# Performance work log

Hardware: AMD Instinct MI355X
Metric: run time of the kernel (lower is better)

## Reference

```python
import jax, jax.numpy as jnp
import numpy as np

N, F_IN, H, W = 8192, 512, 256, 64
THRESHOLD = 0.8


def setup_inputs() -> dict:
    key = jax.random.key(0)
    ks = jax.random.split(key, 9)
    def lin(k, fan_in, shape):
        return (jax.random.normal(k, shape, jnp.float32) / np.sqrt(fan_in)).astype(jnp.float32)
    return {
        "state_batch": jax.random.normal(ks[0], (N, F_IN), jnp.float32),
        "W1": lin(ks[1], F_IN, (F_IN, H)), "b1": jnp.zeros((H,), jnp.float32),
        "W2": lin(ks[2], H, (H, H)),      "b2": jnp.zeros((H,), jnp.float32),
        "Wq": lin(ks[3], H, (H, W)),      "bq": jnp.zeros((W,), jnp.float32),
        "Wh": lin(ks[4], W, (W, 1)),      "bh": jnp.zeros((1,), jnp.float32),
    }


def reference(state_batch, W1, b1, W2, b2, Wq, bq, Wh, bh):
    # classical encoder: two ReLU Linear layers
    enc = jax.nn.relu(state_batch @ W1 + b1)
    enc = jax.nn.relu(enc @ W2 + b2)
    # quantum layer surrogate: bounded features in [-1, 1] like PauliZ expectations
    q_out = jnp.tanh(enc @ Wq + bq)                      # [N, W]

    # pairwise squared-cosine fidelity (vectorized Gram matrix, replaces
    # the itertools.combinations + .item() host-sync loop)
    qn = q_out / (jnp.linalg.norm(q_out, axis=1, keepdims=True) + 1e-12)
    fid = (qn @ qn.T) ** 2                               # [N, N]

    n = q_out.shape[0]
    # graph edges: fid >= threshold, no self loops; edge weight = 1.0
    mask = (fid >= THRESHOLD) & (~jnp.eye(n, dtype=bool))
    deg = mask.sum(axis=1)
    wsum = mask.astype(q_out.dtype).sum(axis=1)          # all weights are 1.0
    # mean neighbor weight; nodes with no neighbors keep their own feature (factor 1)
    mean_w = jnp.where(deg > 0, wsum / jnp.maximum(deg, 1).astype(q_out.dtype), 1.0)
    attn = q_out * mean_w[:, None]                       # [N, W]

    agg = attn.sum(axis=0, keepdims=True)                # [1, W]
    out = (agg @ Wh + bh).squeeze(-1)                    # [1]
    return out
```

## Files before the change

### kernel.cpp

```cpp
#include <hip/hip_runtime.h>
#include <hip/hip_bf16.h>
#include <math.h>


#define N_ROWS 8192
#define F_IN   512
#define H_DIM  256
#define W_DIM  64

#define LDS_S 520
#define LDE   264

#define W1_FRAGS (16 * 16 * 64)
#define W2_FRAGS (16 * 8 * 64)
#define WQ_FRAGS (4 * 8 * 64)
#define PREP_T   (W1_FRAGS + W2_FRAGS + WQ_FRAGS)
#define PREP_BLOCKS ((PREP_T + 255) / 256)

using bf16x8 = __attribute__((ext_vector_type(8))) short;
using bf16x4 = __attribute__((ext_vector_type(4))) short;
using f32x4  = __attribute__((ext_vector_type(4))) float;
typedef __hip_bfloat16 bf16;

__device__ __forceinline__ void split2(float v, bf16& hi, bf16& lo) {
    bf16 h = __float2bfloat16(v);
    hi = h;
    lo = __float2bfloat16(v - __bfloat162float(h));
}

__global__ __launch_bounds__(256) void prep_w(
    const float* __restrict__ W1, const float* __restrict__ W2,
    const float* __restrict__ Wq, const float* __restrict__ bh,
    bf16* __restrict__ W1h, bf16* __restrict__ W1l,
    bf16* __restrict__ W2h, bf16* __restrict__ W2l,
    bf16* __restrict__ Wqh, bf16* __restrict__ Wql,
    float* __restrict__ out)
{
    if (blockIdx.x == 0 && threadIdx.x == 0) out[0] = bh[0];
    int gid = blockIdx.x * 256 + threadIdx.x;
    if (gid < W1_FRAGS) {
        const int l = gid & 63, ks = (gid >> 6) & 15, n16 = gid >> 10;
        const int n = n16 * 16 + (l & 15);
        const int kb = ks * 32 + ((l >> 4) << 3);
        bf16 hb[8], lb[8];
        #pragma unroll
        for (int j = 0; j < 8; ++j)
            split2(W1[(size_t)(kb + j) * H_DIM + n], hb[j], lb[j]);
        *(bf16x8*)(W1h + (size_t)gid * 8) = *(const bf16x8*)hb;
        *(bf16x8*)(W1l + (size_t)gid * 8) = *(const bf16x8*)lb;
        return;
    }
    gid -= W1_FRAGS;
    if (gid < W2_FRAGS) {
        const int l = gid & 63, ks = (gid >> 6) & 7, n16 = gid >> 9;
        const int n = n16 * 16 + (l & 15);
        const int kb = ks * 32 + ((l >> 4) << 3);
        bf16 hb[8], lb[8];
        #pragma unroll
        for (int j = 0; j < 8; ++j)
            split2(W2[(size_t)(kb + j) * H_DIM + n], hb[j], lb[j]);
        *(bf16x8*)(W2h + (size_t)gid * 8) = *(const bf16x8*)hb;
        *(bf16x8*)(W2l + (size_t)gid * 8) = *(const bf16x8*)lb;
        return;
    }
    gid -= W2_FRAGS;
    if (gid < WQ_FRAGS) {
        const int l = gid & 63, ks = (gid >> 6) & 7, n16 = gid >> 9;
        const int n = n16 * 16 + (l & 15);
        const int kb = ks * 32 + ((l >> 4) << 3);
        bf16 hb[8], lb[8];
        #pragma unroll
        for (int j = 0; j < 8; ++j)
            split2(Wq[(size_t)(kb + j) * W_DIM + n], hb[j], lb[j]);
        *(bf16x8*)(Wqh + (size_t)gid * 8) = *(const bf16x8*)hb;
        *(bf16x8*)(Wql + (size_t)gid * 8) = *(const bf16x8*)lb;
    }
}

__global__ __launch_bounds__(512) void fused_chain(
    const float* __restrict__ S,
    const bf16* __restrict__ W1h, const bf16* __restrict__ W1l,
    const bf16* __restrict__ W2h, const bf16* __restrict__ W2l,
    const bf16* __restrict__ Wqh, const bf16* __restrict__ Wql,
    const float* __restrict__ b1, const float* __restrict__ b2,
    const float* __restrict__ bq, const float* __restrict__ Wh,
    float* __restrict__ out)
{
    __shared__ bf16 Ssh[32 * LDS_S];
    __shared__ bf16 Ssl[32 * LDS_S];
    __shared__ bf16 E1h[32 * LDE];
    __shared__ bf16 E1l[32 * LDE];
    __shared__ bf16 E2h[32 * LDE];
    __shared__ bf16 E2l[32 * LDE];
    __shared__ float red[2][64];

    const int t = threadIdx.x;
    const int lane = t & 63;
    const int w = t >> 6, quad = lane >> 4, m16 = t & 15;
    const int row0 = blockIdx.x * 32;

    #pragma unroll
    for (int i = 0; i < 8; ++i) {
        const int idx = i * 2048 + t * 4;
        const int r = idx >> 9, c = idx & 511;
        float4 sv = *(const float4*)(S + (size_t)(row0 + r) * F_IN + c);
        bf16 hb[4], lb[4];
        split2(sv.x, hb[0], lb[0]); split2(sv.y, hb[1], lb[1]);
        split2(sv.z, hb[2], lb[2]); split2(sv.w, hb[3], lb[3]);
        *(bf16x4*)&Ssh[r * LDS_S + c] = *(const bf16x4*)hb;
        *(bf16x4*)&Ssl[r * LDS_S + c] = *(const bf16x4*)lb;
    }

    f32x4 acc[2][2] = {};
    {
        bf16x8 rh[4][2], rl[4][2];
        #pragma unroll
        for (int p = 0; p < 3; ++p)
            #pragma unroll
            for (int jj = 0; jj < 2; ++jj) {
                const size_t off = ((size_t)(((2 * w + jj) * 16 + p) * 64 + lane)) * 8;
                rh[p][jj] = *(const bf16x8*)(W1h + off);
                rl[p][jj] = *(const bf16x8*)(W1l + off);
            }
        __syncthreads();
        #pragma unroll
        for (int ks = 0; ks < 16; ++ks) {
            const int cur = ks & 3;
            if (ks + 3 < 16) {
                const int nx = (ks + 3) & 3;
                #pragma unroll
                for (int jj = 0; jj < 2; ++jj) {
                    const size_t off = ((size_t)(((2 * w + jj) * 16 + ks + 3) * 64 + lane)) * 8;
                    rh[nx][jj] = *(const bf16x8*)(W1h + off);
                    rl[nx][jj] = *(const bf16x8*)(W1l + off);
                }
            }
            const int ao = ks * 32 + quad * 8;
            bf16x8 a0h = *(const bf16x8*)&Ssh[m16 * LDS_S + ao];
            bf16x8 a0l = *(const bf16x8*)&Ssl[m16 * LDS_S + ao];
            bf16x8 a1h = *(const bf16x8*)&Ssh[(16 + m16) * LDS_S + ao];
            bf16x8 a1l = *(const bf16x8*)&Ssl[(16 + m16) * LDS_S + ao];
            #pragma unroll
            for (int jj = 0; jj < 2; ++jj) {
                bf16x8 b_h = rh[cur][jj], b_l = rl[cur][jj];
                acc[0][jj] = __builtin_amdgcn_mfma_f32_16x16x32_bf16(a0h, b_h, acc[0][jj], 0, 0, 0);
                acc[0][jj] = __builtin_amdgcn_mfma_f32_16x16x32_bf16(a0l, b_h, acc[0][jj], 0, 0, 0);
                acc[0][jj] = __builtin_amdgcn_mfma_f32_16x16x32_bf16(a0h, b_l, acc[0][jj], 0, 0, 0);
                acc[1][jj] = __builtin_amdgcn_mfma_f32_16x16x32_bf16(a1h, b_h, acc[1][jj], 0, 0, 0);
                acc[1][jj] = __builtin_amdgcn_mfma_f32_16x16x32_bf16(a1l, b_h, acc[1][jj], 0, 0, 0);
                acc[1][jj] = __builtin_amdgcn_mfma_f32_16x16x32_bf16(a1h, b_l, acc[1][jj], 0, 0, 0);
            }
        }
    }
    #pragma unroll
    for (int i = 0; i < 2; ++i)
        #pragma unroll
        for (int jj = 0; jj < 2; ++jj) {
            const int c = 32 * w + jj * 16 + m16;
            const float bv = b1[c];
            #pragma unroll
            for (int r = 0; r < 4; ++r) {
                const int rr = i * 16 + quad * 4 + r;
                float vv = fmaxf(acc[i][jj][r] + bv, 0.0f);
                split2(vv, E1h[rr * LDE + c], E1l[rr * LDE + c]);
            }
        }

    {
        bf16x8 rh[4][2], rl[4][2];
        #pragma unroll
        for (int p = 0; p < 3; ++p)
            #pragma unroll
            for (int jj = 0; jj < 2; ++jj) {
                const size_t off = ((size_t)(((2 * w + jj) * 8 + p) * 64 + lane)) * 8;
                rh[p][jj] = *(const bf16x8*)(W2h + off);
                rl[p][jj] = *(const bf16x8*)(W2l + off);
            }
        __syncthreads();
        #pragma unroll
        for (int i = 0; i < 2; ++i)
            #pragma unroll
            for (int jj = 0; jj < 2; ++jj)
                acc[i][jj] = (f32x4){0.f, 0.f, 0.f, 0.f};
        #pragma unroll
        for (int ks = 0; ks < 8; ++ks) {
            const int cur = ks & 3;
            if (ks + 3 < 8) {
                const int nx = (ks + 3) & 3;
                #pragma unroll
                for (int jj = 0; jj < 2; ++jj) {
                    const size_t off = ((size_t)(((2 * w + jj) * 8 + ks + 3) * 64 + lane)) * 8;
                    rh[nx][jj] = *(const bf16x8*)(W2h + off);
                    rl[nx][jj] = *(const bf16x8*)(W2l + off);
                }
            }
            const int ao = ks * 32 + quad * 8;
            bf16x8 a0h = *(const bf16x8*)&E1h[m16 * LDE + ao];
            bf16x8 a0l = *(const bf16x8*)&E1l[m16 * LDE + ao];
            bf16x8 a1h = *(const bf16x8*)&E1h[(16 + m16) * LDE + ao];
            bf16x8 a1l = *(const bf16x8*)&E1l[(16 + m16) * LDE + ao];
            #pragma unroll
            for (int jj = 0; jj < 2; ++jj) {
                bf16x8 b_h = rh[cur][jj], b_l = rl[cur][jj];
                acc[0][jj] = __builtin_amdgcn_mfma_f32_16x16x32_bf16(a0h, b_h, acc[0][jj], 0, 0, 0);
                acc[0][jj] = __builtin_amdgcn_mfma_f32_16x16x32_bf16(a0l, b_h, acc[0][jj], 0, 0, 0);
                acc[0][jj] = __builtin_amdgcn_mfma_f32_16x16x32_bf16(a0h, b_l, acc[0][jj], 0, 0, 0);
                acc[1][jj] = __builtin_amdgcn_mfma_f32_16x16x32_bf16(a1h, b_h, acc[1][jj], 0, 0, 0);
                acc[1][jj] = __builtin_amdgcn_mfma_f32_16x16x32_bf16(a1l, b_h, acc[1][jj], 0, 0, 0);
                acc[1][jj] = __builtin_amdgcn_mfma_f32_16x16x32_bf16(a1h, b_l, acc[1][jj], 0, 0, 0);
            }
        }
    }
    #pragma unroll
    for (int i = 0; i < 2; ++i)
        #pragma unroll
        for (int jj = 0; jj < 2; ++jj) {
            const int c = 32 * w + jj * 16 + m16;
            const float bv = b2[c];
            #pragma unroll
            for (int r = 0; r < 4; ++r) {
                const int rr = i * 16 + quad * 4 + r;
                float vv = fmaxf(acc[i][jj][r] + bv, 0.0f);
                split2(vv, E2h[rr * LDE + c], E2l[rr * LDE + c]);
            }
        }

    {
        const int rf = w >> 2, cf = w & 3;
        bf16x8 rh[4], rl[4];
        #pragma unroll
        for (int p = 0; p < 3; ++p) {
            const size_t off = ((size_t)((cf * 8 + p) * 64 + lane)) * 8;
            rh[p] = *(const bf16x8*)(Wqh + off);
            rl[p] = *(const bf16x8*)(Wql + off);
        }
        __syncthreads();
        f32x4 acc3 = {0.f, 0.f, 0.f, 0.f};
        #pragma unroll
        for (int ks = 0; ks < 8; ++ks) {
            const int cur = ks & 3;
            if (ks + 3 < 8) {
                const int nx = (ks + 3) & 3;
                const size_t off = ((size_t)((cf * 8 + ks + 3) * 64 + lane)) * 8;
                rh[nx] = *(const bf16x8*)(Wqh + off);
                rl[nx] = *(const bf16x8*)(Wql + off);
            }
            const int ao = ks * 32 + quad * 8;
            bf16x8 a_h = *(const bf16x8*)&E2h[(rf * 16 + m16) * LDE + ao];
            bf16x8 a_l = *(const bf16x8*)&E2l[(rf * 16 + m16) * LDE + ao];
            acc3 = __builtin_amdgcn_mfma_f32_16x16x32_bf16(a_h, rh[cur], acc3, 0, 0, 0);
            acc3 = __builtin_amdgcn_mfma_f32_16x16x32_bf16(a_l, rh[cur], acc3, 0, 0, 0);
            acc3 = __builtin_amdgcn_mfma_f32_16x16x32_bf16(a_h, rl[cur], acc3, 0, 0, 0);
        }
        const int c = cf * 16 + m16;
        const float bv = bq[c];
        float v = 0.f;
        #pragma unroll
        for (int r = 0; r < 4; ++r)
            v += tanhf(acc3[r] + bv);
        v += __shfl_xor(v, 16, 64);
        v += __shfl_xor(v, 32, 64);
        if (quad == 0) red[rf][c] = v;
        __syncthreads();
        if (t < W_DIM) {
            float s = (red[0][t] + red[1][t]) * Wh[t];
            #pragma unroll
            for (int o = 32; o > 0; o >>= 1) s += __shfl_down(s, o);
            if (t == 0) atomicAdd(out, s);
        }
    }
}

extern "C" void kernel_launch(void* const* d_in, const int* in_sizes, int n_in,
                              void* d_out, int out_size, void* d_ws, size_t ws_size,
                              hipStream_t stream) {
    const float* state = (const float*)d_in[0];
    const float* W1    = (const float*)d_in[1];
    const float* b1    = (const float*)d_in[2];
    const float* W2    = (const float*)d_in[3];
    const float* b2    = (const float*)d_in[4];
    const float* Wq    = (const float*)d_in[5];
    const float* bq    = (const float*)d_in[6];
    const float* Wh    = (const float*)d_in[7];
    const float* bh    = (const float*)d_in[8];

    bf16* p = (bf16*)d_ws;
    bf16* W1h = p; p += (size_t)H_DIM * F_IN;
    bf16* W1l = p; p += (size_t)H_DIM * F_IN;
    bf16* W2h = p; p += (size_t)H_DIM * H_DIM;
    bf16* W2l = p; p += (size_t)H_DIM * H_DIM;
    bf16* Wqh = p; p += (size_t)W_DIM * H_DIM;
    bf16* Wql = p; p += (size_t)W_DIM * H_DIM;

    prep_w<<<PREP_BLOCKS, 256, 0, stream>>>(
        W1, W2, Wq, bh, W1h, W1l, W2h, W2l, Wqh, Wql, (float*)d_out);

    fused_chain<<<N_ROWS / 32, 512, 0, stream>>>(
        state, W1h, W1l, W2h, W2l, Wqh, Wql, b1, b2, bq, Wh, (float*)d_out);
}
```

Before: 96.18 us.

## Split input staging in two halves to overlap conversion with first-layer MFMAs

The state tile is now loaded into registers up front, and the hi/lo split into LDS happens in two column halves. The first half is written before the first barrier. The second half is converted and stored right after that barrier, and the first eight k-steps of the W1 GEMM run on the first half before a second barrier. The aim is to hide global-load latency and conversion work behind MFMA work. The cost is an extra barrier and higher register pressure from holding 8 float4 values.

```diff
diff --git a/kernel.cpp b/kernel.cpp
--- a/kernel.cpp
+++ b/kernel.cpp
@@ -99,16 +99,18 @@
     const int w = t >> 6, quad = lane >> 4, m16 = t & 15;
     const int row0 = blockIdx.x * 32;
 
+    float4 va[4], vb[4];
     #pragma unroll
-    for (int i = 0; i < 8; ++i) {
-        const int idx = i * 2048 + t * 4;
-        const int r = idx >> 9, c = idx & 511;
-        float4 sv = *(const float4*)(S + (size_t)(row0 + r) * F_IN + c);
-        bf16 hb[4], lb[4];
-        split2(sv.x, hb[0], lb[0]); split2(sv.y, hb[1], lb[1]);
-        split2(sv.z, hb[2], lb[2]); split2(sv.w, hb[3], lb[3]);
-        *(bf16x4*)&Ssh[r * LDS_S + c] = *(const bf16x4*)hb;
-        *(bf16x4*)&Ssl[r * LDS_S + c] = *(const bf16x4*)lb;
+    for (int i = 0; i < 4; ++i) {
+        const int idx2 = i * 512 + t;
+        const int r = idx2 >> 6, c = (idx2 & 63) << 2;
+        va[i] = *(const float4*)(S + (size_t)(row0 + r) * F_IN + c);
+    }
+    #pragma unroll
+    for (int i = 0; i < 4; ++i) {
+        const int idx2 = i * 512 + t;
+        const int r = idx2 >> 6, c = 256 + ((idx2 & 63) << 2);
+        vb[i] = *(const float4*)(S + (size_t)(row0 + r) * F_IN + c);
     }
 
     f32x4 acc[2][2] = {};
@@ -122,9 +124,58 @@
                 rh[p][jj] = *(const bf16x8*)(W1h + off);
                 rl[p][jj] = *(const bf16x8*)(W1l + off);
             }
-        __syncthreads();
-        #pragma unroll
-        for (int ks = 0; ks < 16; ++ks) {
+        #pragma unroll
+        for (int i = 0; i < 4; ++i) {
+            const int idx2 = i * 512 + t;
+            const int r = idx2 >> 6, c = (idx2 & 63) << 2;
+            bf16 hb[4], lb[4];
+            split2(va[i].x, hb[0], lb[0]); split2(va[i].y, hb[1], lb[1]);
+            split2(va[i].z, hb[2], lb[2]); split2(va[i].w, hb[3], lb[3]);
+            *(bf16x4*)&Ssh[r * LDS_S + c] = *(const bf16x4*)hb;
+            *(bf16x4*)&Ssl[r * LDS_S + c] = *(const bf16x4*)lb;
+        }
+        __syncthreads();
+        #pragma unroll
+        for (int i = 0; i < 4; ++i) {
+            const int idx2 = i * 512 + t;
+            const int r = idx2 >> 6, c = 256 + ((idx2 & 63) << 2);
+            bf16 hb[4], lb[4];
+            split2(vb[i].x, hb[0], lb[0]); split2(vb[i].y, hb[1], lb[1]);
+            split2(vb[i].z, hb[2], lb[2]); split2(vb[i].w, hb[3], lb[3]);
+            *(bf16x4*)&Ssh[r * LDS_S + c] = *(const bf16x4*)hb;
+            *(bf16x4*)&Ssl[r * LDS_S + c] = *(const bf16x4*)lb;
+        }
+        #pragma unroll
+        for (int ks = 0; ks < 8; ++ks) {
+            const int cur = ks & 3;
+            {
+                const int nx = (ks + 3) & 3;
+                #pragma unroll
+                for (int jj = 0; jj < 2; ++jj) {
+                    const size_t off = ((size_t)(((2 * w + jj) * 16 + ks + 3) * 64 + lane)) * 8;
+                    rh[nx][jj] = *(const bf16x8*)(W1h + off);
+                    rl[nx][jj] = *(const bf16x8*)(W1l + off);
+                }
+            }
+            const int ao = ks * 32 + quad * 8;
+            bf16x8 a0h = *(const bf16x8*)&Ssh[m16 * LDS_S + ao];
+            bf16x8 a0l = *(const bf16x8*)&Ssl[m16 * LDS_S + ao];
+            bf16x8 a1h = *(const bf16x8*)&Ssh[(16 + m16) * LDS_S + ao];
+            bf16x8 a1l = *(const bf16x8*)&Ssl[(16 + m16) * LDS_S + ao];
+            #pragma unroll
+            for (int jj = 0; jj < 2; ++jj) {
+                bf16x8 b_h = rh[cur][jj], b_l = rl[cur][jj];
+                acc[0][jj] = __builtin_amdgcn_mfma_f32_16x16x32_bf16(a0h, b_h, acc[0][jj], 0, 0, 0);
+                acc[0][jj] = __builtin_amdgcn_mfma_f32_16x16x32_bf16(a0l, b_h, acc[0][jj], 0, 0, 0);
+                acc[0][jj] = __builtin_amdgcn_mfma_f32_16x16x32_bf16(a0h, b_l, acc[0][jj], 0, 0, 0);
+                acc[1][jj] = __builtin_amdgcn_mfma_f32_16x16x32_bf16(a1h, b_h, acc[1][jj], 0, 0, 0);
+                acc[1][jj] = __builtin_amdgcn_mfma_f32_16x16x32_bf16(a1l, b_h, acc[1][jj], 0, 0, 0);
+                acc[1][jj] = __builtin_amdgcn_mfma_f32_16x16x32_bf16(a1h, b_l, acc[1][jj], 0, 0, 0);
+            }
+        }
+        __syncthreads();
+        #pragma unroll
+        for (int ks = 8; ks < 16; ++ks) {
             const int cur = ks & 3;
             if (ks + 3 < 16) {
                 const int nx = (ks + 3) & 3;
```

Result: faster. 93.70 us (-2.6%).

## Stream state-tile conversion into LDS in chunks overlapped with layer-1 MFMA loop

Applied to the files above, without the earlier changes.

The fused chain kernel now issues all global loads of the 32x512 state tile up front into registers, then splits and writes them to LDS in four column chunks. The writes are interleaved with the first layer's k-loop, each guarded by an extra barrier, so MFMA work on earlier chunks can start before the whole tile is converted. The weight prep kernel also launches twice as many threads, each handling four elements instead of eight, to expose more parallelism. The cost is more live registers (eight float4 per thread) and additional __syncthreads in the main loop.

```diff
diff --git a/kernel.cpp b/kernel.cpp
--- a/kernel.cpp
+++ b/kernel.cpp
@@ -14,7 +14,7 @@
 #define W1_FRAGS (16 * 16 * 64)
 #define W2_FRAGS (16 * 8 * 64)
 #define WQ_FRAGS (4 * 8 * 64)
-#define PREP_T   (W1_FRAGS + W2_FRAGS + WQ_FRAGS)
+#define PREP_T   ((W1_FRAGS + W2_FRAGS + WQ_FRAGS) * 2)
 #define PREP_BLOCKS ((PREP_T + 255) / 256)
 
 using bf16x8 = __attribute__((ext_vector_type(8))) short;
@@ -37,43 +37,45 @@
     float* __restrict__ out)
 {
     if (blockIdx.x == 0 && threadIdx.x == 0) out[0] = bh[0];
-    int gid = blockIdx.x * 256 + threadIdx.x;
+    int tid = blockIdx.x * 256 + threadIdx.x;
+    const int jh = tid & 1;
+    int gid = tid >> 1;
     if (gid < W1_FRAGS) {
         const int l = gid & 63, ks = (gid >> 6) & 15, n16 = gid >> 10;
         const int n = n16 * 16 + (l & 15);
-        const int kb = ks * 32 + ((l >> 4) << 3);
-        bf16 hb[8], lb[8];
-        #pragma unroll
-        for (int j = 0; j < 8; ++j)
+        const int kb = ks * 32 + ((l >> 4) << 3) + jh * 4;
+        bf16 hb[4], lb[4];
+        #pragma unroll
+        for (int j = 0; j < 4; ++j)
             split2(W1[(size_t)(kb + j) * H_DIM + n], hb[j], lb[j]);
-        *(bf16x8*)(W1h + (size_t)gid * 8) = *(const bf16x8*)hb;
-        *(bf16x8*)(W1l + (size_t)gid * 8) = *(const bf16x8*)lb;
+        *(bf16x4*)(W1h + (size_t)gid * 8 + jh * 4) = *(const bf16x4*)hb;
+        *(bf16x4*)(W1l + (size_t)gid * 8 + jh * 4) = *(const bf16x4*)lb;
         return;
     }
     gid -= W1_FRAGS;
     if (gid < W2_FRAGS) {
         const int l = gid & 63, ks = (gid >> 6) & 7, n16 = gid >> 9;
         const int n = n16 * 16 + (l & 15);
-        const int kb = ks * 32 + ((l >> 4) << 3);
-        bf16 hb[8], lb[8];
-        #pragma unroll
-        for (int j = 0; j < 8; ++j)
+        const int kb = ks * 32 + ((l >> 4) << 3) + jh * 4;
+        bf16 hb[4], lb[4];
+        #pragma unroll
+        for (int j = 0; j < 4; ++j)
             split2(W2[(size_t)(kb + j) * H_DIM + n], hb[j], lb[j]);
-        *(bf16x8*)(W2h + (size_t)gid * 8) = *(const bf16x8*)hb;
-        *(bf16x8*)(W2l + (size_t)gid * 8) = *(const bf16x8*)lb;
+        *(bf16x4*)(W2h + (size_t)gid * 8 + jh * 4) = *(const bf16x4*)hb;
+        *(bf16x4*)(W2l + (size_t)gid * 8 + jh * 4) = *(const bf16x4*)lb;
         return;
     }
     gid -= W2_FRAGS;
     if (gid < WQ_FRAGS) {
         const int l = gid & 63, ks = (gid >> 6) & 7, n16 = gid >> 9;
         const int n = n16 * 16 + (l & 15);
-        const int kb = ks * 32 + ((l >> 4) << 3);
-        bf16 hb[8], lb[8];
-        #pragma unroll
-        for (int j = 0; j < 8; ++j)
+        const int kb = ks * 32 + ((l >> 4) << 3) + jh * 4;
+        bf16 hb[4], lb[4];
+        #pragma unroll
+        for (int j = 0; j < 4; ++j)
             split2(Wq[(size_t)(kb + j) * W_DIM + n], hb[j], lb[j]);
-        *(bf16x8*)(Wqh + (size_t)gid * 8) = *(const bf16x8*)hb;
-        *(bf16x8*)(Wql + (size_t)gid * 8) = *(const bf16x8*)lb;
+        *(bf16x4*)(Wqh + (size_t)gid * 8 + jh * 4) = *(const bf16x4*)hb;
+        *(bf16x4*)(Wql + (size_t)gid * 8 + jh * 4) = *(const bf16x4*)lb;
     }
 }
 
@@ -99,16 +101,30 @@
     const int w = t >> 6, quad = lane >> 4, m16 = t & 15;
     const int row0 = blockIdx.x * 32;
 
+    float4 vs[4][2];
     #pragma unroll
-    for (int i = 0; i < 8; ++i) {
-        const int idx = i * 2048 + t * 4;
-        const int r = idx >> 9, c = idx & 511;
-        float4 sv = *(const float4*)(S + (size_t)(row0 + r) * F_IN + c);
-        bf16 hb[4], lb[4];
-        split2(sv.x, hb[0], lb[0]); split2(sv.y, hb[1], lb[1]);
-        split2(sv.z, hb[2], lb[2]); split2(sv.w, hb[3], lb[3]);
-        *(bf16x4*)&Ssh[r * LDS_S + c] = *(const bf16x4*)hb;
-        *(bf16x4*)&Ssl[r * LDS_S + c] = *(const bf16x4*)lb;
+    for (int ch = 0; ch < 4; ++ch)
+        #pragma unroll
+        for (int i = 0; i < 2; ++i) {
+            const int idx2 = i * 512 + t;
+            const int r = idx2 >> 5, c = ch * 128 + ((idx2 & 31) << 2);
+            vs[ch][i] = *(const float4*)(S + (size_t)(row0 + r) * F_IN + c);
+        }
+
+#define S_WRITE_CHUNK(ch)                                                     \
+    {                                                                         \
+        _Pragma("unroll")                                                     \
+        for (int i = 0; i < 2; ++i) {                                         \
+            const int idx2 = i * 512 + t;                                     \
+            const int r = idx2 >> 5, c = (ch) * 128 + ((idx2 & 31) << 2);     \
+            bf16 hb[4], lb[4];                                                \
+            split2(vs[ch][i].x, hb[0], lb[0]);                                \
+            split2(vs[ch][i].y, hb[1], lb[1]);                                \
+            split2(vs[ch][i].z, hb[2], lb[2]);                                \
+            split2(vs[ch][i].w, hb[3], lb[3]);                                \
+            *(bf16x4*)&Ssh[r * LDS_S + c] = *(const bf16x4*)hb;               \
+            *(bf16x4*)&Ssl[r * LDS_S + c] = *(const bf16x4*)lb;               \
+        }                                                                     \
     }
 
     f32x4 acc[2][2] = {};
@@ -122,9 +138,21 @@
                 rh[p][jj] = *(const bf16x8*)(W1h + off);
                 rl[p][jj] = *(const bf16x8*)(W1l + off);
             }
+        S_WRITE_CHUNK(0)
         __syncthreads();
+        S_WRITE_CHUNK(1)
+
         #pragma unroll
         for (int ks = 0; ks < 16; ++ks) {
+            if (ks == 4) {
+                __syncthreads();
+                S_WRITE_CHUNK(2)
+            } else if (ks == 8) {
+                __syncthreads();
+                S_WRITE_CHUNK(3)
+            } else if (ks == 12) {
+                __syncthreads();
+            }
             const int cur = ks & 3;
             if (ks + 3 < 16) {
                 const int nx = (ks + 3) & 3;
```

Result: faster. 91.73 us (-4.6%).
